# Optimization experiments

Measured on AMD Instinct MI355X. Metric: run time of the kernel, lower is better.

Reference implementation:

```python
import jax, jax.numpy as jnp
import numpy as np


def setup_inputs() -> dict:
    key = jax.random.key(0)
    kq, kk, kv, kb = jax.random.split(key, 4)
    B, H, S, D = 2, 12, 2048, 64
    q = jax.random.normal(kq, (B, H, S, D), dtype=jnp.float32)
    k = jax.random.normal(kk, (B, H, S, D), dtype=jnp.float32)
    v = jax.random.normal(kv, (B, H, S, D), dtype=jnp.float32)
    # sorted block ids -> contiguous blocks along the sequence
    block_ids = jnp.sort(jax.random.randint(kb, (B, S), 0, 4), axis=-1)
    return {"q": q, "k": k, "v": v, "block_ids": block_ids}


def _ghostmax(scores):
    # softmax over [scores, 0]: an extra ghost logit of value 0
    m = jnp.maximum(jnp.max(scores, axis=-1, keepdims=True), 0.0)
    e = jnp.exp(scores - m)
    denom = jnp.sum(e, axis=-1, keepdims=True) + jnp.exp(-m)
    return e / denom


def reference(q, k, v, block_ids):
    B, H, S, D = q.shape
    scaling = 1.0 / jnp.sqrt(jnp.asarray(D, dtype=q.dtype))
    # [B,H,S,S] scores
    scores = jnp.einsum('bhqd,bhkd->bhqk', q, k) * scaling
    # block-causal mask: attend only within same block AND to past positions
    same_block = block_ids[:, :, None] == block_ids[:, None, :]          # [B,S,S]
    causal = jnp.arange(S)[:, None] >= jnp.arange(S)[None, :]            # [S,S]
    mask = (same_block & causal)[:, None, :, :]                          # [B,1,S,S]
    scores = scores + (1.0 - mask.astype(scores.dtype)) * (-1e9)
    weights = _ghostmax(scores)
    # dropout p=0.0 (eval) -> identity
    return jnp.einsum('bhqk,bhkd->bhqd', weights, v)
```

## Files before the change

### kernel.cpp

```cpp
#include <hip/hip_runtime.h>


constexpr int Bc = 2, Hc = 12, Sc = 2048, Dc = 64;
constexpr int QT    = 16;
constexpr int DSUB  = 16;
constexpr int KTILE = 16;

__device__ __forceinline__ float bf_lo(unsigned u) {
    union { unsigned i; float f; } c; c.i = u << 16; return c.f;
}
__device__ __forceinline__ float bf_hi(unsigned u) {
    union { unsigned i; float f; } c; c.i = u & 0xffff0000u; return c.f;
}
__device__ __forceinline__ void expand_store(float* dst, float4 raw) {
    const unsigned* u = (const unsigned*)&raw;
    float4 a, b;
    a.x = bf_lo(u[0]); a.y = bf_hi(u[0]); a.z = bf_lo(u[1]); a.w = bf_hi(u[1]);
    b.x = bf_lo(u[2]); b.y = bf_hi(u[2]); b.z = bf_lo(u[3]); b.w = bf_hi(u[3]);
    ((float4*)dst)[0] = a;
    ((float4*)dst)[1] = b;
}

__global__ void sniff_dtype(const unsigned* __restrict__ q, int* __restrict__ flag) {
    __shared__ int acc;
    const int tid = threadIdx.x;
    if (tid == 0) acc = 0;
    __syncthreads();
    const unsigned word = q[tid];
    const int e = (word >> 7) & 0xff;
    const bool plausible = (e >= 0x70) && (e <= 0x90);
    const unsigned long long mask = __ballot(plausible);
    if ((tid & 63) == 0) atomicAdd(&acc, __popcll(mask));
    __syncthreads();
    if (tid == 0) *flag = (acc >= 128) ? 1 : 0;
}

template <bool BF16_IN>
__device__ __forceinline__ void attn_body(
    const void* __restrict__ qv, const void* __restrict__ kv_,
    const void* __restrict__ vv, const int* __restrict__ bidg,
    float* __restrict__ outg)
{
    __shared__ __align__(16) float ks[KTILE][Dc];
    __shared__ __align__(16) float vs[KTILE][Dc];
    __shared__ int kb[KTILE];

    const int bh    = blockIdx.x;
    const int qt    = (gridDim.y - 1) - blockIdx.y;
    const int b     = bh / Hc;
    const int tid   = threadIdx.x;
    const int q0    = qt * QT;
    const int r     = q0 + (tid >> 2);
    const int dbase = (tid & 3) * DSUB;

    const int* brow   = bidg + b * Sc;
    const int  my_bid = brow[r];
    const int  bid0   = brow[q0];

    int lo = 0, hi = q0;
    while (lo < hi) {
        int mid = (lo + hi) >> 1;
        if (brow[mid] < bid0) lo = mid + 1; else hi = mid;
    }
    const int kstart = lo & ~(KTILE - 1);
    const int ntiles = (q0 + QT - kstart) / KTILE;

    float qr[DSUB];
    if (BF16_IN) {
        const float4* qraw = (const float4*)((const unsigned short*)qv
                              + ((size_t)bh * Sc + r) * Dc + dbase);
        #pragma unroll
        for (int i = 0; i < 2; ++i) {
            float4 rw = qraw[i];
            const unsigned* u = (const unsigned*)&rw;
            #pragma unroll
            for (int j = 0; j < 4; ++j) {
                qr[i * 8 + 2 * j + 0] = bf_lo(u[j]) * 0.125f;
                qr[i * 8 + 2 * j + 1] = bf_hi(u[j]) * 0.125f;
            }
        }
    } else {
        const float4* qraw = (const float4*)((const float*)qv
                              + ((size_t)bh * Sc + r) * Dc + dbase);
        #pragma unroll
        for (int i = 0; i < 4; ++i) {
            float4 t = qraw[i];
            qr[4*i+0] = t.x * 0.125f; qr[4*i+1] = t.y * 0.125f;
            qr[4*i+2] = t.z * 0.125f; qr[4*i+3] = t.w * 0.125f;
        }
    }

    float o[DSUB];
    #pragma unroll
    for (int d = 0; d < DSUB; ++d) o[d] = 0.f;
    float m = -1e30f;
    float l = 0.f;

    const float4* kbase = BF16_IN
        ? (const float4*)((const unsigned short*)kv_ + (size_t)bh * Sc * Dc)
        : (const float4*)((const float*)kv_ + (size_t)bh * Sc * Dc);
    const float4* vbase = BF16_IN
        ? (const float4*)((const unsigned short*)vv + (size_t)bh * Sc * Dc)
        : (const float4*)((const float*)vv + (size_t)bh * Sc * Dc);
    constexpr int NR    = BF16_IN ? 2 : 4;
    constexpr int ROWF4 = BF16_IN ? 8 : 16;

    float4 kreg[NR], vreg[NR];
    #pragma unroll
    for (int j = 0; j < NR; ++j) {
        kreg[j] = kbase[kstart * ROWF4 + tid + j * 64];
        vreg[j] = vbase[kstart * ROWF4 + tid + j * 64];
    }

    for (int t = 0; t < ntiles; ++t) {
        const int kt = kstart + t * KTILE;

        __syncthreads();
        if (BF16_IN) {
            #pragma unroll
            for (int j = 0; j < NR; ++j) {
                expand_store(&ks[0][0] + 8 * (tid + j * 64), kreg[j]);
                expand_store(&vs[0][0] + 8 * (tid + j * 64), vreg[j]);
            }
        } else {
            float4* kd = (float4*)&ks[0][0];
            float4* vd = (float4*)&vs[0][0];
            #pragma unroll
            for (int j = 0; j < NR; ++j) {
                kd[tid + j * 64] = kreg[j];
                vd[tid + j * 64] = vreg[j];
            }
        }
        if (tid < KTILE) kb[tid] = brow[kt + tid];
        __syncthreads();

        if (t + 1 < ntiles) {
            const int ktn = kt + KTILE;
            #pragma unroll
            for (int j = 0; j < NR; ++j) {
                kreg[j] = kbase[ktn * ROWF4 + tid + j * 64];
                vreg[j] = vbase[ktn * ROWF4 + tid + j * 64];
            }
        }

        float s[KTILE];
        unsigned vmask = 0;
        #pragma unroll
        for (int kk = 0; kk < KTILE; ++kk) {
            const float4* krow4 = (const float4*)(&ks[kk][dbase]);
            float s0 = 0.f, s1 = 0.f, s2 = 0.f, s3 = 0.f;
            #pragma unroll
            for (int i = 0; i < DSUB / 4; ++i) {
                float4 kv4 = krow4[i];
                s0 = fmaf(qr[4*i+0], kv4.x, s0);
                s1 = fmaf(qr[4*i+1], kv4.y, s1);
                s2 = fmaf(qr[4*i+2], kv4.z, s2);
                s3 = fmaf(qr[4*i+3], kv4.w, s3);
            }
            float sv = (s0 + s1) + (s2 + s3);
            sv += __shfl_xor(sv, 1);
            sv += __shfl_xor(sv, 2);

            const int  kgi   = kt + kk;
            const bool valid = (kgi <= r) && (kb[kk] == my_bid);
            vmask |= (valid ? 1u : 0u) << kk;
            s[kk] = valid ? sv : -1e30f;
        }

        float pmax = s[0];
        #pragma unroll
        for (int kk = 1; kk < KTILE; ++kk) pmax = fmaxf(pmax, s[kk]);
        const float M = fmaxf(m, pmax);
        const float c = __expf(m - M);
        l *= c;
        #pragma unroll
        for (int d = 0; d < DSUB; ++d) o[d] *= c;
        m = M;

        #pragma unroll
        for (int kk = 0; kk < KTILE; ++kk) {
            const float e = ((vmask >> kk) & 1u) ? __expf(s[kk] - m) : 0.f;
            l += e;
            s[kk] = e;
        }

        #pragma unroll
        for (int kk = 0; kk < KTILE; ++kk) {
            const float e = s[kk];
            const float4* vrow = (const float4*)(&vs[kk][dbase]);
            #pragma unroll
            for (int i = 0; i < DSUB / 4; ++i) {
                float4 vv4 = vrow[i];
                o[4*i+0] = fmaf(e, vv4.x, o[4*i+0]);
                o[4*i+1] = fmaf(e, vv4.y, o[4*i+1]);
                o[4*i+2] = fmaf(e, vv4.z, o[4*i+2]);
                o[4*i+3] = fmaf(e, vv4.w, o[4*i+3]);
            }
        }
    }

    const float Mg    = fmaxf(m, 0.f);
    const float cg    = __expf(m - Mg);
    const float denom = l * cg + __expf(-Mg);
    const float scale = cg / denom;

    float4* orow = (float4*)(outg + ((size_t)bh * Sc + r) * Dc + dbase);
    #pragma unroll
    for (int i = 0; i < 4; ++i) {
        float4 t;
        t.x = o[4*i+0] * scale; t.y = o[4*i+1] * scale;
        t.z = o[4*i+2] * scale; t.w = o[4*i+3] * scale;
        orow[i] = t;
    }
}

__global__ __launch_bounds__(64, 3) void block_causal_attn(
    const void* __restrict__ qv, const void* __restrict__ kv_,
    const void* __restrict__ vv, const int* __restrict__ bidg,
    float* __restrict__ outg, const int* __restrict__ flag)
{
    if (*flag)
        attn_body<true >(qv, kv_, vv, bidg, outg);
    else
        attn_body<false>(qv, kv_, vv, bidg, outg);
}

extern "C" void kernel_launch(void* const* d_in, const int* in_sizes, int n_in,
                              void* d_out, int out_size, void* d_ws, size_t ws_size,
                              hipStream_t stream) {
    const void* q    = d_in[0];
    const void* k    = d_in[1];
    const void* v    = d_in[2];
    const int*  bids = (const int*)d_in[3];
    float*      out  = (float*)d_out;
    int*        flag = (int*)d_ws;

    sniff_dtype<<<1, 256, 0, stream>>>((const unsigned*)q, flag);
    dim3 grid(Bc * Hc, Sc / QT);
    block_causal_attn<<<grid, dim3(64), 0, stream>>>(q, k, v, bids, out, flag);
}
```

Baseline: 259.7 us.

## Double-buffer K/V tiles in LDS via direct global-to-LDS loads for fp32 path

For fp32 inputs, K and V tiles are now loaded with global_load_lds straight into a double-buffered LDS array. The next tile is prefetched while the current one is computed, replacing the register staging and the per-tile __syncthreads with a single waitcnt. This removes VGPR pressure and barrier overhead in the single-wave block. The launch bounds are loosened to a waves_per_eu range, which lets the compiler choose a different occupancy and register trade-off. LDS use doubles.

```diff
diff --git a/kernel.cpp b/kernel.cpp
--- a/kernel.cpp
+++ b/kernel.cpp
@@ -19,6 +19,12 @@
     b.x = bf_lo(u[2]); b.y = bf_hi(u[2]); b.z = bf_lo(u[3]); b.w = bf_hi(u[3]);
     ((float4*)dst)[0] = a;
     ((float4*)dst)[1] = b;
+}
+
+__device__ __forceinline__ void dma16(const void* g, void* l) {
+    __builtin_amdgcn_global_load_lds(
+        (const __attribute__((address_space(1))) void*)g,
+        (__attribute__((address_space(3))) void*)l, 16, 0, 0);
 }
 
 __global__ void sniff_dtype(const unsigned* __restrict__ q, int* __restrict__ flag) {
@@ -41,9 +47,9 @@
     const void* __restrict__ vv, const int* __restrict__ bidg,
     float* __restrict__ outg)
 {
-    __shared__ __align__(16) float ks[KTILE][Dc];
-    __shared__ __align__(16) float vs[KTILE][Dc];
-    __shared__ int kb[KTILE];
+    __shared__ __align__(16) float ks[2][KTILE][Dc];
+    __shared__ __align__(16) float vs[2][KTILE][Dc];
+    __shared__ int kb[2][KTILE];
 
     const int bh    = blockIdx.x;
     const int qt    = (gridDim.y - 1) - blockIdx.y;
@@ -96,50 +102,50 @@
     float m = -1e30f;
     float l = 0.f;
 
-    const float4* kbase = BF16_IN
-        ? (const float4*)((const unsigned short*)kv_ + (size_t)bh * Sc * Dc)
-        : (const float4*)((const float*)kv_ + (size_t)bh * Sc * Dc);
-    const float4* vbase = BF16_IN
-        ? (const float4*)((const unsigned short*)vv + (size_t)bh * Sc * Dc)
-        : (const float4*)((const float*)vv + (size_t)bh * Sc * Dc);
-    constexpr int NR    = BF16_IN ? 2 : 4;
-    constexpr int ROWF4 = BF16_IN ? 8 : 16;
-
-    float4 kreg[NR], vreg[NR];
-    #pragma unroll
-    for (int j = 0; j < NR; ++j) {
-        kreg[j] = kbase[kstart * ROWF4 + tid + j * 64];
-        vreg[j] = vbase[kstart * ROWF4 + tid + j * 64];
+    const char* kibase = (const char*)((const float*)kv_ + (size_t)bh * Sc * Dc);
+    const char* vibase = (const char*)((const float*)vv  + (size_t)bh * Sc * Dc);
+    const unsigned short* kb16 = (const unsigned short*)kv_ + (size_t)bh * Sc * Dc;
+    const unsigned short* vb16 = (const unsigned short*)vv  + (size_t)bh * Sc * Dc;
+
+    if (!BF16_IN) {
+        const char* gk = kibase + (size_t)kstart * Dc * 4;
+        const char* gv = vibase + (size_t)kstart * Dc * 4;
+        #pragma unroll
+        for (int i = 0; i < 4; ++i) {
+            dma16(gk + i * 1024 + tid * 16, (char*)&ks[0][0][0] + i * 1024);
+            dma16(gv + i * 1024 + tid * 16, (char*)&vs[0][0][0] + i * 1024);
+        }
+        if (tid < KTILE) kb[0][tid] = brow[kstart + tid];
     }
 
     for (int t = 0; t < ntiles; ++t) {
-        const int kt = kstart + t * KTILE;
-
-        __syncthreads();
+        const int kt  = kstart + t * KTILE;
+        const int buf = t & 1;
+
         if (BF16_IN) {
-            #pragma unroll
-            for (int j = 0; j < NR; ++j) {
-                expand_store(&ks[0][0] + 8 * (tid + j * 64), kreg[j]);
-                expand_store(&vs[0][0] + 8 * (tid + j * 64), vreg[j]);
-            }
+            __syncthreads();
+            const float4* kb4 = (const float4*)(kb16 + (size_t)kt * Dc);
+            const float4* vb4 = (const float4*)(vb16 + (size_t)kt * Dc);
+            #pragma unroll
+            for (int j = 0; j < 2; ++j) {
+                expand_store(&ks[buf][0][0] + 8 * (tid + j * 64), kb4[tid + j * 64]);
+                expand_store(&vs[buf][0][0] + 8 * (tid + j * 64), vb4[tid + j * 64]);
+            }
+            if (tid < KTILE) kb[buf][tid] = brow[kt + tid];
+            __syncthreads();
         } else {
-            float4* kd = (float4*)&ks[0][0];
-            float4* vd = (float4*)&vs[0][0];
-            #pragma unroll
-            for (int j = 0; j < NR; ++j) {
-                kd[tid + j * 64] = kreg[j];
-                vd[tid + j * 64] = vreg[j];
-            }
-        }
-        if (tid < KTILE) kb[tid] = brow[kt + tid];
-        __syncthreads();
-
-        if (t + 1 < ntiles) {
-            const int ktn = kt + KTILE;
-            #pragma unroll
-            for (int j = 0; j < NR; ++j) {
-                kreg[j] = kbase[ktn * ROWF4 + tid + j * 64];
-                vreg[j] = vbase[ktn * ROWF4 + tid + j * 64];
+            asm volatile("s_waitcnt vmcnt(0) lgkmcnt(0)" ::: "memory");
+            __builtin_amdgcn_sched_barrier(0);
+            if (t + 1 < ntiles) {
+                const int   ktn = kt + KTILE;
+                const char* gk  = kibase + (size_t)ktn * Dc * 4;
+                const char* gv  = vibase + (size_t)ktn * Dc * 4;
+                #pragma unroll
+                for (int i = 0; i < 4; ++i) {
+                    dma16(gk + i * 1024 + tid * 16, (char*)&ks[buf ^ 1][0][0] + i * 1024);
+                    dma16(gv + i * 1024 + tid * 16, (char*)&vs[buf ^ 1][0][0] + i * 1024);
+                }
+                if (tid < KTILE) kb[buf ^ 1][tid] = brow[ktn + tid];
             }
         }
 
@@ -147,7 +153,7 @@
         unsigned vmask = 0;
         #pragma unroll
         for (int kk = 0; kk < KTILE; ++kk) {
-            const float4* krow4 = (const float4*)(&ks[kk][dbase]);
+            const float4* krow4 = (const float4*)(&ks[buf][kk][dbase]);
             float s0 = 0.f, s1 = 0.f, s2 = 0.f, s3 = 0.f;
             #pragma unroll
             for (int i = 0; i < DSUB / 4; ++i) {
@@ -162,7 +168,7 @@
             sv += __shfl_xor(sv, 2);
 
             const int  kgi   = kt + kk;
-            const bool valid = (kgi <= r) && (kb[kk] == my_bid);
+            const bool valid = (kgi <= r) && (kb[buf][kk] == my_bid);
             vmask |= (valid ? 1u : 0u) << kk;
             s[kk] = valid ? sv : -1e30f;
         }
@@ -187,7 +193,7 @@
         #pragma unroll
         for (int kk = 0; kk < KTILE; ++kk) {
             const float e = s[kk];
-            const float4* vrow = (const float4*)(&vs[kk][dbase]);
+            const float4* vrow = (const float4*)(&vs[buf][kk][dbase]);
             #pragma unroll
             for (int i = 0; i < DSUB / 4; ++i) {
                 float4 vv4 = vrow[i];
@@ -214,7 +220,9 @@
     }
 }
 
-__global__ __launch_bounds__(64, 3) void block_causal_attn(
+__global__ __launch_bounds__(64)
+__attribute__((amdgpu_waves_per_eu(1, 4)))
+void block_causal_attn(
     const void* __restrict__ qv, const void* __restrict__ kv_,
     const void* __restrict__ vv, const int* __restrict__ bidg,
     float* __restrict__ outg, const int* __restrict__ flag)
```

Result: slower. 306.4 us (+18.0%).
